# Performance work log

Measured on AMD Instinct MI355X. Metric: run time of the kernel, lower is better.

## Reference

```python
import jax, jax.numpy as jnp
import numpy as np
import itertools

# --- constants matching init_kwargs / chosen problem size ---
MOD = 6.283185307179586       # 2*pi, modular wrap for angular error
DEG_U = 90.0                  # deg_u
DEG_P = 1.0                   # deg_p (grid resolution in degrees)
D = 4                         # number of active sources (ones per label row)
NUM_CLASSES = 181             # angle grid size
BATCH = 131072

# All D! permutations as one-hot matrices: exact LAP solution by brute force
# (equivalent to lap.lapjv on the square DxD cost matrix).
_PERMS = np.array(list(itertools.permutations(range(D))), dtype=np.int32)   # (D!, D)
PERM_OH = jnp.asarray(np.eye(D, dtype=np.float32)[_PERMS])                  # (D!, D, D)


def setup_inputs() -> dict:
    key = jax.random.key(0)
    k1, k2 = jax.random.split(key)
    # predicted DOAs live in the first D slots of logits (radians)
    logits = jax.random.normal(k1, (BATCH, NUM_CLASSES), dtype=jnp.float32)
    # labels: exactly D ones per row (D distinct grid indices)
    scores = jax.random.uniform(k2, (BATCH, NUM_CLASSES))
    idx = jnp.argsort(scores, axis=1)[:, :D]                     # D distinct cols per row
    labels = jnp.zeros((BATCH, NUM_CLASSES), dtype=jnp.int32)
    labels = labels.at[jnp.arange(BATCH)[:, None], idx].set(1)
    return {"logits": logits, "labels": labels}


def _sq_mod_diff(a, b):
    # ((a - b + mod/2) % mod - mod/2)**2 : squared wrapped angular error
    d = jnp.mod(a - b + MOD / 2, MOD) - MOD / 2
    return d * d


def reference(logits, labels):
    # np.where(labels==1)[0] returns ascending indices of the ones.
    # Stable ascending argsort of a 0/1 row puts the one-indices (in ascending
    # order) in the last D slots.
    one_idx = jnp.argsort(labels, axis=1)[:, -D:]                        # (B, D)
    label_ang = (one_idx.astype(jnp.float32) * DEG_P - DEG_U) * (jnp.pi / 180.0)  # (B, D) radians

    doa = logits[:, :D]                                                  # (B, D)
    # per-sample DxD cost matrix of squared modular errors
    cost = _sq_mod_diff(doa[:, :, None], label_ang[:, None, :])          # (B, D, D)
    # optimal assignment = min total cost over all permutations (exact LAP)
    totals = jnp.einsum('bij,pij->bp', cost, PERM_OH)                    # (B, D!)
    min_total = jnp.min(totals, axis=1)                                  # (B,)
    rmse = jnp.sqrt(min_total / D)                                       # (B,)
    return rmse.mean()
```

## Files before the change

kernel.cpp:

```cpp
#include <hip/hip_runtime.h>
#include <hip/hip_bf16.h>
#include <math.h>

constexpr int   NC      = 181;
constexpr int   BATCH   = 131072;
constexpr float MODC    = 6.2831853071795864769f;
constexpr float HALFMOD = 3.1415926535897932385f;
constexpr float DEG2RAD = 0.017453292519943295f;

constexpr unsigned MAGIC181 = 23729102u;

constexpr int RPB   = 64;
constexpr int WINT4 = RPB * NC / 4;
constexpr int NOPS  = (WINT4 + 63) / 64;
constexpr int OPW   = (NOPS + 3) / 4;

__device__ __forceinline__ float sq_mod_diff(float x) {
    float t = x + HALFMOD;
    float m = t - floorf(t * (1.0f / MODC)) * MODC;
    float d = m - HALFMOD;
    return d * d;
}

__global__ __launch_bounds__(256) void fused_kernel(
    const float* __restrict__ logits,
    const int*   __restrict__ labels,
    float*       __restrict__ out)
{
    __shared__ int4     win[WINT4];
    __shared__ unsigned bm[RPB * 8];

    const int tid  = threadIdx.x;
    const int lane = tid & 63;
    const int w    = tid >> 6;
    const int rowBase = blockIdx.x * RPB;

    bm[tid]       = 0u;
    bm[tid + 256] = 0u;

    float d0 = 0.f, d1 = 0.f, d2 = 0.f, d3 = 0.f;
    if (tid < RPB) {
        const float* lp = logits + (size_t)(rowBase + tid) * NC;
        d0 = lp[0]; d1 = lp[1]; d2 = lp[2]; d3 = lp[3];
    }

    const int4* gbase = (const int4*)labels + (size_t)blockIdx.x * WINT4;
    #pragma unroll
    for (int k = 0; k < OPW; ++k) {
        const int op = w * OPW + k;
        if (op < NOPS) {
            const int x4 = op * 64 + lane;
            if (x4 < WINT4) {
                __builtin_amdgcn_global_load_lds(
                    (const __attribute__((address_space(1))) void*)(gbase + x4),
                    (__attribute__((address_space(3))) void*)(&win[x4]),
                    16, 0, 0);
            }
        }
    }
    __syncthreads();

    #pragma unroll
    for (int k = 0; k < OPW; ++k) {
        const int idx = tid + 256 * k;
        if (idx < WINT4) {
            const int4 v = win[idx];
            if ((v.x | v.y | v.z | v.w) != 0) {
                const unsigned g0 = (unsigned)idx * 4u;
                #pragma unroll
                for (int c = 0; c < 4; ++c) {
                    const int comp = (c == 0) ? v.x : (c == 1) ? v.y
                                   : (c == 2) ? v.z : v.w;
                    if (comp != 0) {
                        const unsigned g   = g0 + (unsigned)c;
                        const unsigned row = __umulhi(g, MAGIC181);
                        const unsigned cls = g - 181u * row;
                        atomicOr(&bm[row * 8u + (cls >> 5u)],
                                 1u << (cls & 31u));
                    }
                }
            }
        }
    }
    __syncthreads();

    if (tid < RPB) {
        const float doa[4] = {d0, d1, d2, d3};

        float ang[4];
        int found = 0;
        #pragma unroll
        for (int k = 0; k < 8; ++k) {
            unsigned mm = bm[tid * 8 + k];
            while (mm) {
                const int j = __builtin_ctz(mm);
                mm &= mm - 1;
                ang[found & 3] = ((float)(k * 32 + j) - 90.0f) * DEG2RAD;
                ++found;
            }
        }

        float cst[4][4];
        #pragma unroll
        for (int i = 0; i < 4; ++i)
            #pragma unroll
            for (int j = 0; j < 4; ++j)
                cst[i][j] = sq_mod_diff(doa[i] - ang[j]);

        float best = 1e30f;
        #pragma unroll
        for (int a = 0; a < 4; ++a) {
            #pragma unroll
            for (int b = 0; b < 4; ++b) {
                if (b == a) continue;
                const float top = cst[0][a] + cst[1][b];
                #pragma unroll
                for (int e = 0; e < 4; ++e) {
                    if (e == a || e == b) continue;
                    const int f = 6 - a - b - e;
                    best = fminf(best, top + cst[2][e] + cst[3][f]);
                }
            }
        }
        float sum = sqrtf(best * 0.25f);

        #pragma unroll
        for (int off = 32; off > 0; off >>= 1)
            sum += __shfl_down(sum, off);
        if (lane == 0)
            atomicAdd(out, sum * (1.0f / (float)BATCH));
    }
}

extern "C" void kernel_launch(void* const* d_in, const int* in_sizes, int n_in,
                              void* d_out, int out_size, void* d_ws, size_t ws_size,
                              hipStream_t stream) {
    const float* logits = (const float*)d_in[0];
    const int*   labels = (const int*)d_in[1];
    float*       out    = (float*)d_out;

    hipMemsetAsync(out, 0, sizeof(float), stream);

    fused_kernel<<<BATCH / RPB, 256, 0, stream>>>(logits, labels, out);
}
```

Measured before the change: 194.3 us.

## Replace LDS-direct label loads with register loads and compact byte masks

Labels are now loaded into registers with ordinary vector global loads instead of global_load_lds into a full int4 LDS window. Each int4 is compressed to a 4-bit nonzero mask stored as one byte in shared memory. The second pass then scans 32-bit words holding 16 columns each and iterates only over the set bits. This cuts LDS footprint, which may raise occupancy, and reduces LDS read traffic, at the cost of more registers for the held loads.

```diff
diff --git a/kernel.cpp b/kernel.cpp
--- a/kernel.cpp
+++ b/kernel.cpp
@@ -12,8 +12,9 @@
 
 constexpr int RPB   = 64;
 constexpr int WINT4 = RPB * NC / 4;
-constexpr int NOPS  = (WINT4 + 63) / 64;
-constexpr int OPW   = (NOPS + 3) / 4;
+constexpr int FULL  = WINT4 / 256;
+constexpr int TAIL  = WINT4 - FULL * 256;
+constexpr int MB4   = WINT4 / 4;
 
 __device__ __forceinline__ float sq_mod_diff(float x) {
     float t = x + HALFMOD;
@@ -27,58 +28,62 @@
     const int*   __restrict__ labels,
     float*       __restrict__ out)
 {
-    __shared__ int4     win[WINT4];
-    __shared__ unsigned bm[RPB * 8];
+    __shared__ unsigned char smask[WINT4];
+    __shared__ unsigned      bm[RPB * 8];
 
     const int tid  = threadIdx.x;
     const int lane = tid & 63;
-    const int w    = tid >> 6;
-    const int rowBase = blockIdx.x * RPB;
 
     bm[tid]       = 0u;
     bm[tid + 256] = 0u;
 
     float d0 = 0.f, d1 = 0.f, d2 = 0.f, d3 = 0.f;
     if (tid < RPB) {
-        const float* lp = logits + (size_t)(rowBase + tid) * NC;
+        const float* lp = logits + (size_t)(blockIdx.x * RPB + tid) * NC;
         d0 = lp[0]; d1 = lp[1]; d2 = lp[2]; d3 = lp[3];
     }
 
     const int4* gbase = (const int4*)labels + (size_t)blockIdx.x * WINT4;
+    int4 v[FULL];
     #pragma unroll
-    for (int k = 0; k < OPW; ++k) {
-        const int op = w * OPW + k;
-        if (op < NOPS) {
-            const int x4 = op * 64 + lane;
-            if (x4 < WINT4) {
-                __builtin_amdgcn_global_load_lds(
-                    (const __attribute__((address_space(1))) void*)(gbase + x4),
-                    (__attribute__((address_space(3))) void*)(&win[x4]),
-                    16, 0, 0);
-            }
-        }
+    for (int k = 0; k < FULL; ++k)
+        v[k] = gbase[tid + 256 * k];
+    int4 vt = {0, 0, 0, 0};
+    if (tid < TAIL) vt = gbase[tid + 256 * FULL];
+
+    __builtin_amdgcn_sched_barrier(0);
+
+    #pragma unroll
+    for (int k = 0; k < FULL; ++k) {
+        const unsigned m = (unsigned)(v[k].x != 0)
+                         | ((unsigned)(v[k].y != 0) << 1)
+                         | ((unsigned)(v[k].z != 0) << 2)
+                         | ((unsigned)(v[k].w != 0) << 3);
+        smask[tid + 256 * k] = (unsigned char)m;
+    }
+    if (tid < TAIL) {
+        const unsigned m = (unsigned)(vt.x != 0)
+                         | ((unsigned)(vt.y != 0) << 1)
+                         | ((unsigned)(vt.z != 0) << 2)
+                         | ((unsigned)(vt.w != 0) << 3);
+        smask[tid + 256 * FULL] = (unsigned char)m;
     }
     __syncthreads();
 
     #pragma unroll
-    for (int k = 0; k < OPW; ++k) {
+    for (int k = 0; k < 3; ++k) {
         const int idx = tid + 256 * k;
-        if (idx < WINT4) {
-            const int4 v = win[idx];
-            if ((v.x | v.y | v.z | v.w) != 0) {
-                const unsigned g0 = (unsigned)idx * 4u;
-                #pragma unroll
-                for (int c = 0; c < 4; ++c) {
-                    const int comp = (c == 0) ? v.x : (c == 1) ? v.y
-                                   : (c == 2) ? v.z : v.w;
-                    if (comp != 0) {
-                        const unsigned g   = g0 + (unsigned)c;
-                        const unsigned row = __umulhi(g, MAGIC181);
-                        const unsigned cls = g - 181u * row;
-                        atomicOr(&bm[row * 8u + (cls >> 5u)],
-                                 1u << (cls & 31u));
-                    }
-                }
+        if (idx < MB4) {
+            unsigned mw = ((const unsigned*)smask)[idx];
+            while (mw) {
+                const int bit = __builtin_ctz(mw);
+                mw &= mw - 1;
+                const unsigned g   = (unsigned)idx * 16u
+                                   + ((unsigned)bit >> 3) * 4u
+                                   + ((unsigned)bit & 7u);
+                const unsigned row = __umulhi(g, MAGIC181);
+                const unsigned cls = g - 181u * row;
+                atomicOr(&bm[row * 8u + (cls >> 5u)], 1u << (cls & 31u));
             }
         }
     }
```

New measurement: 189.1 us. -2.7%, faster.
